# Kernel optimization log

Measured on AMD Instinct MI355X. Metric: run time of the kernel, lower is better.

## Reference

```python
import jax, jax.numpy as jnp
import numpy as np

GROUP_SIZE = 64

def _dequant(wq, scale, zero):
    # HQQ groupwise dequant: W = (Wq - zero) * scale, groups along input dim.
    out_dim, in_dim = wq.shape
    g = in_dim // GROUP_SIZE
    w = (wq.astype(jnp.float32).reshape(out_dim, g, GROUP_SIZE) - zero[:, :, None]) * scale[:, :, None]
    return w.reshape(out_dim, in_dim)

def setup_inputs() -> dict:
    key = jax.random.key(0)
    ks = jax.random.split(key, 10)
    T, H, I = 256, 4096, 14336
    G1, G2 = H // GROUP_SIZE, I // GROUP_SIZE  # 64, 224
    x = jax.random.normal(ks[0], (T, H), dtype=jnp.float32)
    w1_q = jax.random.randint(ks[1], (I, H), 0, 16, dtype=jnp.int32)
    w1_scale = jax.random.uniform(ks[2], (I, G1), dtype=jnp.float32) * 0.02
    w1_zero = jax.random.uniform(ks[3], (I, G1), dtype=jnp.float32) * 8.0
    w3_q = jax.random.randint(ks[4], (I, H), 0, 16, dtype=jnp.int32)
    w3_scale = jax.random.uniform(ks[5], (I, G1), dtype=jnp.float32) * 0.02
    w3_zero = jax.random.uniform(ks[6], (I, G1), dtype=jnp.float32) * 8.0
    w2_q = jax.random.randint(ks[7], (H, I), 0, 16, dtype=jnp.int32)
    w2_scale = jax.random.uniform(ks[8], (H, G2), dtype=jnp.float32) * 0.02
    w2_zero = jax.random.uniform(ks[9], (H, G2), dtype=jnp.float32) * 8.0
    return {"x": x, "w1_q": w1_q, "w1_scale": w1_scale, "w1_zero": w1_zero,
            "w3_q": w3_q, "w3_scale": w3_scale, "w3_zero": w3_zero,
            "w2_q": w2_q, "w2_scale": w2_scale, "w2_zero": w2_zero}

def reference(x, w1_q, w1_scale, w1_zero, w3_q, w3_scale, w3_zero, w2_q, w2_scale, w2_zero):
    w1 = _dequant(w1_q, w1_scale, w1_zero)  # [I, H]
    w3 = _dequant(w3_q, w3_scale, w3_zero)  # [I, H]
    w2 = _dequant(w2_q, w2_scale, w2_zero)  # [H, I]
    gate = jax.nn.silu(jnp.einsum('th,ih->ti', x, w1))  # [T, I]
    up = jnp.einsum('th,ih->ti', x, w3)                 # [T, I]
    return jnp.einsum('ti,hi->th', gate * up, w2)       # [T, H]
```

## Files before the change

### kernel.cpp

```cpp
#include <hip/hip_runtime.h>
#include <cstdint>
#include <cstddef>

#define T_DIM 256
#define H_DIM 4096
#define I_DIM 14336

typedef __attribute__((ext_vector_type(8))) short s8v;
typedef __attribute__((ext_vector_type(4))) float f4v;

static constexpr size_t XS_BYTES   = (size_t)T_DIM * H_DIM * 2;
static constexpr size_t ACT_OFF    = XS_BYTES;
static constexpr size_t ACT_BYTES  = (size_t)T_DIM * I_DIM * 2;
static constexpr size_t PART_OFF   = ACT_OFF + ACT_BYTES;
static constexpr size_t PART_BYTES = 8ull * T_DIM * H_DIM * 4;
static constexpr size_t WS_NEEDED  = PART_OFF + PART_BYTES;

__device__ __forceinline__ unsigned short f2bf(float f) {
    unsigned u = __builtin_bit_cast(unsigned, f);
    u += 0x7fffu + ((u >> 16) & 1u);
    return (unsigned short)(u >> 16);
}

__device__ __forceinline__ s8v dq8(const int4 qa, const int4 qb, float s, float ns) {
    union { unsigned short u[8]; s8v v; } r;
    r.u[0] = f2bf(fmaf((float)qa.x, s, ns));
    r.u[1] = f2bf(fmaf((float)qa.y, s, ns));
    r.u[2] = f2bf(fmaf((float)qa.z, s, ns));
    r.u[3] = f2bf(fmaf((float)qa.w, s, ns));
    r.u[4] = f2bf(fmaf((float)qb.x, s, ns));
    r.u[5] = f2bf(fmaf((float)qb.y, s, ns));
    r.u[6] = f2bf(fmaf((float)qb.z, s, ns));
    r.u[7] = f2bf(fmaf((float)qb.w, s, ns));
    return r.v;
}

__global__ __launch_bounds__(256) void k_prep(const float* __restrict__ x,
                                              unsigned short* __restrict__ xs) {
    int gs   = blockIdx.x * 256 + threadIdx.x;
    int kt   = gs >> 11;
    int rem  = gs & 2047;
    int row  = rem >> 3;
    int slot = rem & 7;
    const float* xp = x + (size_t)row * H_DIM + kt * 64 + slot * 8;
    float4 a = *(const float4*)xp;
    float4 b = *(const float4*)(xp + 4);
    union { unsigned short u[8]; s8v v; } r;
    r.u[0] = f2bf(a.x); r.u[1] = f2bf(a.y); r.u[2] = f2bf(a.z); r.u[3] = f2bf(a.w);
    r.u[4] = f2bf(b.x); r.u[5] = f2bf(b.y); r.u[6] = f2bf(b.z); r.u[7] = f2bf(b.w);
    *(s8v*)(xs + (size_t)kt * 16384 + (size_t)row * 64 + (size_t)slot * 8) = r.v;
}

struct P1 { int4 x0, x1, x2, x3, q1a, q1b, q3a, q3b; float s1, z1, s3, z3; };

__global__ __launch_bounds__(512, 2) void k_gemm1(
    const int* __restrict__ w1q, const float* __restrict__ w1s, const float* __restrict__ w1z,
    const int* __restrict__ w3q, const float* __restrict__ w3s, const float* __restrict__ w3z,
    const unsigned short* __restrict__ xs, unsigned short* __restrict__ act)
{
    __shared__ unsigned char lds[2][49152];
    const int tid  = threadIdx.x;
    const int blk  = blockIdx.x;
    const int n0   = blk * 64;
    const int wid  = tid >> 6;
    const int lane = tid & 63;
    const int wr   = wid >> 1;
    const int wc   = wid & 1;
    const int lr   = lane & 15;
    const int lkb  = lane >> 4;
    const int aswz = (lr & 7) << 4;

    const int sr = tid >> 3, sl = tid & 7;
    const int sbyte = sr * 128 + ((sl * 16) ^ ((sr & 7) << 4));
    const int4*  xbase = (const int4*)xs;
    const size_t wrow  = (size_t)(n0 + sr) * H_DIM;
    const float* s1p = w1s + (size_t)(n0 + sr) * 64;
    const float* z1p = w1z + (size_t)(n0 + sr) * 64;
    const float* s3p = w3s + (size_t)(n0 + sr) * 64;
    const float* z3p = w3z + (size_t)(n0 + sr) * 64;

    f4v accg[4][2], accu[4][2];
    const f4v fz = {0.f, 0.f, 0.f, 0.f};
    #pragma unroll
    for (int i = 0; i < 4; ++i)
        #pragma unroll
        for (int j = 0; j < 2; ++j) { accg[i][j] = fz; accu[i][j] = fz; }

    auto load = [&](int kt, P1& p) {
        const int4* xp = xbase + kt * 2048 + sr * 8 + sl;
        p.x0 = xp[0]; p.x1 = xp[512]; p.x2 = xp[1024]; p.x3 = xp[1536];
        const int4* p1 = (const int4*)(w1q + wrow + kt * 64 + sl * 8);
        const int4* p3 = (const int4*)(w3q + wrow + kt * 64 + sl * 8);
        p.q1a = p1[0]; p.q1b = p1[1]; p.q3a = p3[0]; p.q3b = p3[1];
        p.s1 = s1p[kt]; p.z1 = z1p[kt]; p.s3 = s3p[kt]; p.z3 = z3p[kt];
    };
    auto store = [&](const P1& p, unsigned char* b) {
        *(int4*)(b + sbyte)         = p.x0;
        *(int4*)(b + sbyte + 8192)  = p.x1;
        *(int4*)(b + sbyte + 16384) = p.x2;
        *(int4*)(b + sbyte + 24576) = p.x3;
        *(s8v*)(b + 32768 + sbyte) = dq8(p.q1a, p.q1b, p.s1, -p.z1 * p.s1);
        *(s8v*)(b + 40960 + sbyte) = dq8(p.q3a, p.q3b, p.s3, -p.z3 * p.s3);
    };
    auto compute = [&](const unsigned char* b) {
        #pragma unroll
        for (int kf = 0; kf < 2; ++kf) {
            const int kb = (kf * 64 + lkb * 16) ^ aswz;
            s8v a[4];
            #pragma unroll
            for (int mf = 0; mf < 4; ++mf)
                a[mf] = *(const s8v*)(b + (wr * 64 + mf * 16 + lr) * 128 + kb);
            s8v b1[2], b3[2];
            #pragma unroll
            for (int nf = 0; nf < 2; ++nf) {
                const int rbo = (wc * 32 + nf * 16 + lr) * 128 + kb;
                b1[nf] = *(const s8v*)(b + 32768 + rbo);
                b3[nf] = *(const s8v*)(b + 40960 + rbo);
            }
            #pragma unroll
            for (int mf = 0; mf < 4; ++mf)
                #pragma unroll
                for (int nf = 0; nf < 2; ++nf) {
                    accg[mf][nf] = __builtin_amdgcn_mfma_f32_16x16x32_bf16(a[mf], b1[nf], accg[mf][nf], 0, 0, 0);
                    accu[mf][nf] = __builtin_amdgcn_mfma_f32_16x16x32_bf16(a[mf], b3[nf], accu[mf][nf], 0, 0, 0);
                }
        }
    };

    P1 A, B;
    load(0, A);
    store(A, lds[0]);
    load(1, B);
    __syncthreads();

    for (int it = 0; it < 32; ++it) {
        const int t = it * 2;
        load(t + 2 > 63 ? 63 : t + 2, A);
        compute(lds[0]);
        __syncthreads();
        store(B, lds[1]);
        __syncthreads();
        load(t + 3 > 63 ? 63 : t + 3, B);
        compute(lds[1]);
        __syncthreads();
        store(A, lds[0]);
        __syncthreads();
    }

    unsigned char* actb = (unsigned char*)act + (size_t)blk * 32768;
    #pragma unroll
    for (int mf = 0; mf < 4; ++mf)
        #pragma unroll
        for (int nf = 0; nf < 2; ++nf)
            #pragma unroll
            for (int r = 0; r < 4; ++r) {
                const int m  = wr * 64 + mf * 16 + lkb * 4 + r;
                const int nl = wc * 32 + nf * 16 + lr;
                float g = accg[mf][nf][r];
                float u = accu[mf][nf][r];
                float sg = g / (1.0f + __expf(-g));
                *(unsigned short*)(actb + m * 128 + nl * 2) = f2bf(sg * u);
            }
}

struct P2 { int4 a0, a1, a2, a3, q0, q1, q2, q3; float s2, z2; };

template<bool ATOMIC>
__global__ __launch_bounds__(512, 2) void k_gemm2(
    const int* __restrict__ w2q, const float* __restrict__ w2s, const float* __restrict__ w2z,
    const unsigned short* __restrict__ act, float* __restrict__ outp)
{
    __shared__ unsigned char lds[2][49152];
    const int tid  = threadIdx.x;
    const int nb   = blockIdx.x & 31;
    const int kc   = blockIdx.x >> 5;
    const int n0   = nb * 128;
    const int wid  = tid >> 6;
    const int lane = tid & 63;
    const int wr   = wid >> 2;
    const int wc   = wid & 3;
    const int lr   = lane & 15;
    const int lkb  = lane >> 4;
    const int aswz = (lr & 7) << 4;

    const int sr = tid >> 3, sl = tid & 7;
    const int abyte = sr * 128 + ((sl * 16) ^ ((sr & 7) << 4));
    const int r2 = tid >> 2, sq = tid & 3;
    const int wb0 = r2 * 128 + (((sq * 2) * 16)     ^ ((r2 & 7) << 4));
    const int wb1 = r2 * 128 + (((sq * 2 + 1) * 16) ^ ((r2 & 7) << 4));
    const int4*  abase = (const int4*)act;
    const size_t w2row = (size_t)(n0 + r2) * I_DIM;
    const float* s2p = w2s + (size_t)(n0 + r2) * 224;
    const float* z2p = w2z + (size_t)(n0 + r2) * 224;

    f4v acc[8][2];
    const f4v fz = {0.f, 0.f, 0.f, 0.f};
    #pragma unroll
    for (int i = 0; i < 8; ++i) { acc[i][0] = fz; acc[i][1] = fz; }

    auto load = [&](int kt, P2& p) {
        const int4* ap = abase + kt * 2048 + sr * 8 + sl;
        p.a0 = ap[0]; p.a1 = ap[512]; p.a2 = ap[1024]; p.a3 = ap[1536];
        const int4* wp = (const int4*)(w2q + w2row + kt * 64 + sq * 16);
        p.q0 = wp[0]; p.q1 = wp[1]; p.q2 = wp[2]; p.q3 = wp[3];
        p.s2 = s2p[kt]; p.z2 = z2p[kt];
    };
    auto store = [&](const P2& p, unsigned char* b) {
        *(int4*)(b + abyte)         = p.a0;
        *(int4*)(b + abyte + 8192)  = p.a1;
        *(int4*)(b + abyte + 16384) = p.a2;
        *(int4*)(b + abyte + 24576) = p.a3;
        float ns = -p.z2 * p.s2;
        *(s8v*)(b + 32768 + wb0) = dq8(p.q0, p.q1, p.s2, ns);
        *(s8v*)(b + 32768 + wb1) = dq8(p.q2, p.q3, p.s2, ns);
    };
    auto compute = [&](const unsigned char* b) {
        #pragma unroll
        for (int kf = 0; kf < 2; ++kf) {
            const int kb = (kf * 64 + lkb * 16) ^ aswz;
            s8v bfr[2];
            #pragma unroll
            for (int nf = 0; nf < 2; ++nf)
                bfr[nf] = *(const s8v*)(b + 32768 + (wc * 32 + nf * 16 + lr) * 128 + kb);
            #pragma unroll
            for (int mf = 0; mf < 8; ++mf) {
                s8v a = *(const s8v*)(b + (wr * 128 + mf * 16 + lr) * 128 + kb);
                acc[mf][0] = __builtin_amdgcn_mfma_f32_16x16x32_bf16(a, bfr[0], acc[mf][0], 0, 0, 0);
                acc[mf][1] = __builtin_amdgcn_mfma_f32_16x16x32_bf16(a, bfr[1], acc[mf][1], 0, 0, 0);
            }
        }
    };

    const int kt0 = kc * 28;
    P2 A, B;
    load(kt0, A);
    store(A, lds[0]);
    load(kt0 + 1, B);
    __syncthreads();

    for (int it = 0; it < 14; ++it) {
        const int t = it * 2;
        load(kt0 + (t + 2 > 27 ? 27 : t + 2), A);
        compute(lds[0]);
        __syncthreads();
        store(B, lds[1]);
        __syncthreads();
        load(kt0 + (t + 3 > 27 ? 27 : t + 3), B);
        compute(lds[1]);
        __syncthreads();
        store(A, lds[0]);
        __syncthreads();
    }

    float* pout = outp + (ATOMIC ? 0 : (size_t)kc * ((size_t)T_DIM * H_DIM));
    #pragma unroll
    for (int mf = 0; mf < 8; ++mf)
        #pragma unroll
        for (int nf = 0; nf < 2; ++nf)
            #pragma unroll
            for (int r = 0; r < 4; ++r) {
                const int m = wr * 128 + mf * 16 + lkb * 4 + r;
                const int n = n0 + wc * 32 + nf * 16 + lr;
                if (ATOMIC) atomicAdd(&outp[(size_t)m * H_DIM + n], acc[mf][nf][r]);
                else        pout[(size_t)m * H_DIM + n] = acc[mf][nf][r];
            }
}

__global__ __launch_bounds__(256) void k_reduce(const f4v* __restrict__ p,
                                                f4v* __restrict__ o) {
    int i = blockIdx.x * 256 + threadIdx.x;
    f4v s = p[i];
    #pragma unroll
    for (int c = 1; c < 8; ++c) s += p[(size_t)c * 262144 + i];
    o[i] = s;
}

__global__ __launch_bounds__(256) void k_zero(f4v* __restrict__ o) {
    o[blockIdx.x * 256 + threadIdx.x] = (f4v){0.f, 0.f, 0.f, 0.f};
}

extern "C" void kernel_launch(void* const* d_in, const int* in_sizes, int n_in,
                              void* d_out, int out_size, void* d_ws, size_t ws_size,
                              hipStream_t stream) {
    const float* x   = (const float*)d_in[0];
    const int*   w1q = (const int*)  d_in[1];
    const float* w1s = (const float*)d_in[2];
    const float* w1z = (const float*)d_in[3];
    const int*   w3q = (const int*)  d_in[4];
    const float* w3s = (const float*)d_in[5];
    const float* w3z = (const float*)d_in[6];
    const int*   w2q = (const int*)  d_in[7];
    const float* w2s = (const float*)d_in[8];
    const float* w2z = (const float*)d_in[9];
    float* outp = (float*)d_out;

    unsigned short* xs  = (unsigned short*)d_ws;
    unsigned short* act = (unsigned short*)((char*)d_ws + ACT_OFF);
    float*          prt = (float*)((char*)d_ws + PART_OFF);
    const bool partials = (ws_size >= WS_NEEDED);

    k_prep<<<512, 256, 0, stream>>>(x, xs);
    k_gemm1<<<224, 512, 0, stream>>>(w1q, w1s, w1z, w3q, w3s, w3z, xs, act);
    if (partials) {
        k_gemm2<false><<<256, 512, 0, stream>>>(w2q, w2s, w2z, act, prt);
        k_reduce<<<1024, 256, 0, stream>>>((const f4v*)prt, (f4v*)outp);
    } else {
        k_zero<<<1024, 256, 0, stream>>>((f4v*)outp);
        k_gemm2<true><<<256, 512, 0, stream>>>(w2q, w2s, w2z, act, outp);
    }
}
```

Before: 296.7 us.

## Replace syncthreads with lightweight LDS barriers and relax launch-bound occupancy hint

Swaps __syncthreads for custom barriers. Read-side barriers skip waiting on outstanding memory counters, so in-flight global prefetch loads are not drained. Write-side barriers wait only on lgkmcnt before s_barrier. It also drops the minimum-2-blocks-per-CU hint, giving the compiler more registers per thread. The intent is to keep global loads overlapping compute across barriers, at the risk of lower occupancy and scheduling changes from the sched_barrier fences.

New measurement: 298.5 us. About the same (+0.6%).

```diff
diff --git a/kernel.cpp b/kernel.cpp
--- a/kernel.cpp
+++ b/kernel.cpp
@@ -20,6 +20,18 @@
     unsigned u = __builtin_bit_cast(unsigned, f);
     u += 0x7fffu + ((u >> 16) & 1u);
     return (unsigned short)(u >> 16);
+}
+
+__device__ __forceinline__ void bar_read() {
+    __builtin_amdgcn_sched_barrier(0);
+    __builtin_amdgcn_s_barrier();
+    __builtin_amdgcn_sched_barrier(0);
+}
+__device__ __forceinline__ void bar_write() {
+    __builtin_amdgcn_sched_barrier(0);
+    asm volatile("s_waitcnt lgkmcnt(0)" ::: "memory");
+    __builtin_amdgcn_s_barrier();
+    __builtin_amdgcn_sched_barrier(0);
 }
 
 __device__ __forceinline__ s8v dq8(const int4 qa, const int4 qb, float s, float ns) {
@@ -53,7 +65,7 @@
 
 struct P1 { int4 x0, x1, x2, x3, q1a, q1b, q3a, q3b; float s1, z1, s3, z3; };
 
-__global__ __launch_bounds__(512, 2) void k_gemm1(
+__global__ __launch_bounds__(512) void k_gemm1(
     const int* __restrict__ w1q, const float* __restrict__ w1s, const float* __restrict__ w1z,
     const int* __restrict__ w3q, const float* __restrict__ w3s, const float* __restrict__ w3z,
     const unsigned short* __restrict__ xs, unsigned short* __restrict__ act)
@@ -131,20 +143,20 @@
     load(0, A);
     store(A, lds[0]);
     load(1, B);
-    __syncthreads();
+    bar_write();
 
     for (int it = 0; it < 32; ++it) {
         const int t = it * 2;
         load(t + 2 > 63 ? 63 : t + 2, A);
         compute(lds[0]);
-        __syncthreads();
+        bar_read();
         store(B, lds[1]);
-        __syncthreads();
+        bar_write();
         load(t + 3 > 63 ? 63 : t + 3, B);
         compute(lds[1]);
-        __syncthreads();
+        bar_read();
         store(A, lds[0]);
-        __syncthreads();
+        bar_write();
     }
 
     unsigned char* actb = (unsigned char*)act + (size_t)blk * 32768;
@@ -166,7 +178,7 @@
 struct P2 { int4 a0, a1, a2, a3, q0, q1, q2, q3; float s2, z2; };
 
 template<bool ATOMIC>
-__global__ __launch_bounds__(512, 2) void k_gemm2(
+__global__ __launch_bounds__(512) void k_gemm2(
     const int* __restrict__ w2q, const float* __restrict__ w2s, const float* __restrict__ w2z,
     const unsigned short* __restrict__ act, float* __restrict__ outp)
 {
@@ -236,20 +248,20 @@
     load(kt0, A);
     store(A, lds[0]);
     load(kt0 + 1, B);
-    __syncthreads();
+    bar_write();
 
     for (int it = 0; it < 14; ++it) {
         const int t = it * 2;
         load(kt0 + (t + 2 > 27 ? 27 : t + 2), A);
         compute(lds[0]);
-        __syncthreads();
+        bar_read();
         store(B, lds[1]);
-        __syncthreads();
+        bar_write();
         load(kt0 + (t + 3 > 27 ? 27 : t + 3), B);
         compute(lds[1]);
-        __syncthreads();
+        bar_read();
         store(A, lds[0]);
-        __syncthreads();
+        bar_write();
     }
 
     float* pout = outp + (ATOMIC ? 0 : (size_t)kc * ((size_t)T_DIM * H_DIM));
```
